# Optimization experiments

Measured on AMD Instinct MI355X. Metric: run time of the kernel, lower is better.

The kernel has to match this reference:

```python
import jax, jax.numpy as jnp
import numpy as np

T, B, OBS, ENC, H, A = 128, 256, 512, 256, 512, 18
N = T * B


def setup_inputs() -> dict:
    key = jax.random.key(0)
    ks = jax.random.split(key, 16)
    s = 0.02
    return {
        "x": jax.random.normal(ks[0], (N, OBS), jnp.float32),
        "gru_state": jax.random.normal(ks[1], (1, B, H), jnp.float32),
        "done": (jax.random.uniform(ks[2], (N,)) < 0.05).astype(jnp.float32),
        "action": jax.random.randint(ks[3], (N,), 0, A),
        # encoder MLP
        "w1": jax.random.normal(ks[4], (ENC, OBS), jnp.float32) * s,
        "b1": jnp.zeros((ENC,), jnp.float32),
        "w2": jax.random.normal(ks[5], (ENC, ENC), jnp.float32) * s,
        "b2": jnp.zeros((ENC,), jnp.float32),
        # GRU (PyTorch layout: gates [r, z, n] stacked along dim 0)
        "w_ih": jax.random.normal(ks[6], (3 * H, ENC), jnp.float32) * s,
        "w_hh": jax.random.normal(ks[7], (3 * H, H), jnp.float32) * s,
        "b_ih": jnp.zeros((3 * H,), jnp.float32),
        "b_hh": jnp.zeros((3 * H,), jnp.float32),
        # heads
        "w_actor": jax.random.normal(ks[8], (A, H), jnp.float32) * 0.01,
        "b_actor": jnp.zeros((A,), jnp.float32),
        "w_critic": jax.random.normal(ks[9], (1, H), jnp.float32) * s,
        "b_critic": jnp.zeros((1,), jnp.float32),
    }


def _gru_agent(x, gru_state, done, action, w1, b1, w2, b2, w_ih, w_hh, b_ih, b_hh,
               w_actor, b_actor, w_critic, b_critic):
    # MLP encoder
    h = jax.nn.relu(x @ w1.T + b1)
    h = jax.nn.relu(h @ w2.T + b2)  # (N, ENC)
    b = gru_state.shape[1]
    hs = h.reshape(-1, b, h.shape[-1])      # (T, B, ENC)
    dn = done.reshape(-1, b)                # (T, B)
    # precompute input-side gates for all timesteps: (T, B, 3H)
    gx = jnp.einsum('tbi,gi->tbg', hs, w_ih) + b_ih

    def step(h_prev, inp):
        gx_t, d_t = inp
        h_prev = h_prev * (1.0 - d_t)[:, None]   # done-based reset
        gh = h_prev @ w_hh.T + b_hh
        xr, xz, xn = jnp.split(gx_t, 3, axis=-1)
        hr, hz, hn = jnp.split(gh, 3, axis=-1)
        r = jax.nn.sigmoid(xr + hr)
        z = jax.nn.sigmoid(xz + hz)
        n = jnp.tanh(xn + r * hn)
        h_new = (1.0 - z) * n + z * h_prev
        return h_new, h_new

    h_last, outs = jax.lax.scan(step, gru_state[0], (gx, dn))
    hidden = outs.reshape(-1, outs.shape[-1])   # (N, H)

    logits = hidden @ w_actor.T + b_actor
    logp = jax.nn.log_softmax(logits, axis=-1)
    log_prob = jnp.take_along_axis(logp, action[:, None], axis=1)[:, 0]
    entropy = -jnp.sum(jnp.exp(logp) * logp, axis=-1)
    value = hidden @ w_critic.T + b_critic       # (N, 1)
    return log_prob, entropy, value, h_last[None]


def reference(x, gru_state, done, action, w1, b1, w2, b2, w_ih, w_hh, b_ih, b_hh,
              w_actor, b_actor, w_critic, b_critic):
    return _gru_agent(x, gru_state, done, action, w1, b1, w2, b2, w_ih, w_hh,
                      b_ih, b_hh, w_actor, b_actor, w_critic, b_critic)
```

## Files before the change

kernel.cpp:

```cpp
#include <hip/hip_runtime.h>
#include <hip/hip_bf16.h>

typedef short bf16x8 __attribute__((ext_vector_type(8)));
typedef float f32x4 __attribute__((ext_vector_type(4)));
typedef unsigned short u16;
typedef unsigned int u32;
typedef unsigned long long u64;

#define AS1 __attribute__((address_space(1)))
#define AS3 __attribute__((address_space(3)))

__device__ __forceinline__ u16 f2bf(float f) {
    __hip_bfloat16 h = __float2bfloat16(f);
    u16 r;
    __builtin_memcpy(&r, &h, 2);
    return r;
}
__device__ __forceinline__ float bf2f(u16 u) {
    u32 v = ((u32)u) << 16;
    float f;
    __builtin_memcpy(&f, &v, 4);
    return f;
}


constexpr int NW1  = 256 * 512;
constexpr int NW2  = 256 * 256;
constexpr int NWIH = 1536 * 256;

__global__ __launch_bounds__(256) void prep_kernel(
    const float* __restrict__ w1, const float* __restrict__ w2,
    const float* __restrict__ wih, const float* __restrict__ wact,
    const float* __restrict__ wcrit,
    u16* __restrict__ w1b, u16* __restrict__ w2b,
    u16* __restrict__ wihb, u16* __restrict__ wcatb) {
    long long gid = (long long)blockIdx.x * 256 + threadIdx.x;
    long long i4 = gid * 4;
    const float* src;
    u16* dst;
    if (i4 < NW1) { src = w1; dst = w1b; }
    else if ((i4 -= NW1) < NW2) { src = w2; dst = w2b; }
    else if ((i4 -= NW2) < NWIH) { src = wih; dst = wihb; }
    else {
        i4 -= NWIH;
        #pragma unroll
        for (int e = 0; e < 4; e++) {
            long long idx = i4 + e;
            int row = (int)(idx >> 9), col = (int)(idx & 511);
            float v = (row < 18) ? wact[row * 512 + col]
                    : (row == 18 ? wcrit[col] : 0.f);
            wcatb[idx] = f2bf(v);
        }
        return;
    }
    float4 v = *reinterpret_cast<const float4*>(src + i4);
    uint2 p;
    p.x = (u32)f2bf(v.x) | ((u32)f2bf(v.y) << 16);
    p.y = (u32)f2bf(v.z) | ((u32)f2bf(v.w) << 16);
    *reinterpret_cast<uint2*>(dst + i4) = p;
}

__global__ __launch_bounds__(256) void gemm_a32_bt_kernel(
    const float* __restrict__ A, const u16* __restrict__ B,
    const float* __restrict__ bias, u16* __restrict__ out,
    int M, int N, int K) {
    __shared__ u16 As[128 * 64];
    __shared__ u16 Bs[128 * 64];
    int tid = threadIdx.x;
    int lane = tid & 63, wave = tid >> 6;
    int m16 = lane & 15, quad = lane >> 4;
    int nb = N >> 7;
    int bm = blockIdx.x / nb, bn = blockIdx.x % nb;
    int wm = wave >> 1, wn = wave & 1;

    f32x4 acc[4][4];
    #pragma unroll
    for (int i = 0; i < 4; i++)
        #pragma unroll
        for (int j = 0; j < 4; j++) acc[i][j] = (f32x4){0.f, 0.f, 0.f, 0.f};

    const int rbase = wave * 32 + (lane >> 3);
    const int cpr = lane & 7;
    const int ar = tid >> 1, ah = (tid & 1) * 32;
    int kiters = K >> 6;
    for (int kb = 0; kb < kiters; kb++) {
        #pragma unroll
        for (int i = 0; i < 4; i++) {
            int r = rbase + i * 8;
            int cg = cpr ^ (r & 7);
            const u16* gb_ = B + (long long)(bn * 128 + r) * K + kb * 64 + cg * 8;
            __builtin_amdgcn_global_load_lds((const AS1 u32*)gb_, (AS3 u32*)&Bs[r * 64 + cpr * 8], 16, 0, 0);
        }
        const float* ga = A + (long long)(bm * 128 + ar) * K + kb * 64 + ah;
        #pragma unroll
        for (int g = 0; g < 4; g++) {
            float4 v0 = *reinterpret_cast<const float4*>(ga + g * 8);
            float4 v1 = *reinterpret_cast<const float4*>(ga + g * 8 + 4);
            uint4 pk;
            pk.x = (u32)f2bf(v0.x) | ((u32)f2bf(v0.y) << 16);
            pk.y = (u32)f2bf(v0.z) | ((u32)f2bf(v0.w) << 16);
            pk.z = (u32)f2bf(v1.x) | ((u32)f2bf(v1.y) << 16);
            pk.w = (u32)f2bf(v1.z) | ((u32)f2bf(v1.w) << 16);
            int sc = ((ah >> 3) + g) ^ (ar & 7);
            *reinterpret_cast<uint4*>(&As[ar * 64 + sc * 8]) = pk;
        }
        __syncthreads();
        #pragma unroll
        for (int ks = 0; ks < 2; ks++) {
            bf16x8 af[4], bfr[4];
            int lc = ks * 4 + quad;
            #pragma unroll
            for (int mt = 0; mt < 4; mt++) {
                int m = wm * 64 + mt * 16 + m16;
                af[mt] = *reinterpret_cast<const bf16x8*>(&As[m * 64 + (lc ^ (m & 7)) * 8]);
            }
            #pragma unroll
            for (int nt = 0; nt < 4; nt++) {
                int n = wn * 64 + nt * 16 + m16;
                bfr[nt] = *reinterpret_cast<const bf16x8*>(&Bs[n * 64 + (lc ^ (n & 7)) * 8]);
            }
            #pragma unroll
            for (int mt = 0; mt < 4; mt++)
                #pragma unroll
                for (int nt = 0; nt < 4; nt++)
                    acc[mt][nt] = __builtin_amdgcn_mfma_f32_16x16x32_bf16(af[mt], bfr[nt], acc[mt][nt], 0, 0, 0);
        }
        __syncthreads();
    }
    #pragma unroll
    for (int nt = 0; nt < 4; nt++) {
        int n = bn * 128 + wn * 64 + nt * 16 + m16;
        float bv = bias[n];
        #pragma unroll
        for (int mt = 0; mt < 4; mt++) {
            #pragma unroll
            for (int i = 0; i < 4; i++) {
                int m = bm * 128 + wm * 64 + mt * 16 + quad * 4 + i;
                float v = acc[mt][nt][i] + bv;
                out[(long long)m * N + n] = f2bf(fmaxf(v, 0.f));
            }
        }
    }
}

__global__ __launch_bounds__(256) void gemm_bt_kernel(
    const u16* __restrict__ A, const u16* __restrict__ B,
    const float* __restrict__ bias, u16* __restrict__ out,
    int M, int N, int K, int mode) {
    __shared__ u16 As[128 * 64];
    __shared__ u16 Bs[128 * 64];
    int tid = threadIdx.x;
    int lane = tid & 63, wave = tid >> 6;
    int m16 = lane & 15, quad = lane >> 4;
    int nb = N >> 7;
    int bm = blockIdx.x / nb, bn = blockIdx.x % nb;
    int wm = wave >> 1, wn = wave & 1;

    f32x4 acc[4][4];
    #pragma unroll
    for (int i = 0; i < 4; i++)
        #pragma unroll
        for (int j = 0; j < 4; j++) acc[i][j] = (f32x4){0.f, 0.f, 0.f, 0.f};

    const int rbase = wave * 32 + (lane >> 3);
    const int cpr = lane & 7;
    int kiters = K >> 6;
    for (int kb = 0; kb < kiters; kb++) {
        #pragma unroll
        for (int i = 0; i < 4; i++) {
            int r = rbase + i * 8;
            int cg = cpr ^ (r & 7);
            const u16* ga = A + (long long)(bm * 128 + r) * K + kb * 64 + cg * 8;
            const u16* gb_ = B + (long long)(bn * 128 + r) * K + kb * 64 + cg * 8;
            __builtin_amdgcn_global_load_lds((const AS1 u32*)ga, (AS3 u32*)&As[r * 64 + cpr * 8], 16, 0, 0);
            __builtin_amdgcn_global_load_lds((const AS1 u32*)gb_, (AS3 u32*)&Bs[r * 64 + cpr * 8], 16, 0, 0);
        }
        __syncthreads();
        #pragma unroll
        for (int ks = 0; ks < 2; ks++) {
            bf16x8 af[4], bfr[4];
            int lc = ks * 4 + quad;
            #pragma unroll
            for (int mt = 0; mt < 4; mt++) {
                int m = wm * 64 + mt * 16 + m16;
                af[mt] = *reinterpret_cast<const bf16x8*>(&As[m * 64 + (lc ^ (m & 7)) * 8]);
            }
            #pragma unroll
            for (int nt = 0; nt < 4; nt++) {
                int n = wn * 64 + nt * 16 + m16;
                bfr[nt] = *reinterpret_cast<const bf16x8*>(&Bs[n * 64 + (lc ^ (n & 7)) * 8]);
            }
            #pragma unroll
            for (int mt = 0; mt < 4; mt++)
                #pragma unroll
                for (int nt = 0; nt < 4; nt++)
                    acc[mt][nt] = __builtin_amdgcn_mfma_f32_16x16x32_bf16(af[mt], bfr[nt], acc[mt][nt], 0, 0, 0);
        }
        __syncthreads();
    }
    if (mode == 0) {
        #pragma unroll
        for (int nt = 0; nt < 4; nt++) {
            int n = bn * 128 + wn * 64 + nt * 16 + m16;
            float bv = bias[n];
            #pragma unroll
            for (int mt = 0; mt < 4; mt++) {
                #pragma unroll
                for (int i = 0; i < 4; i++) {
                    int m = bm * 128 + wm * 64 + mt * 16 + quad * 4 + i;
                    float v = acc[mt][nt][i] + bv;
                    out[(long long)m * N + n] = f2bf(fmaxf(v, 0.f));
                }
            }
        }
    } else {
        #pragma unroll
        for (int nt = 0; nt < 4; nt++) {
            int n = bn * 128 + wn * 64 + nt * 16 + m16;
            float bv = bias[n];
            int gkind = n >> 9, gj = n & 511;
            int gu = gj >> 5;
            int gate_local = gkind * 32 + (gj & 31);
            #pragma unroll
            for (int mt = 0; mt < 4; mt++) {
                #pragma unroll
                for (int i = 0; i < 4; i++) {
                    int m = bm * 128 + wm * 64 + mt * 16 + quad * 4 + i;
                    int t = m >> 8, bg = m & 255;
                    long long dst = ((((long long)t * 16 + (bg >> 4)) * 16 + gu) * 16 + (bg & 15)) * 96 + gate_local;
                    out[dst] = f2bf(acc[mt][nt][i] + bv);
                }
            }
        }
    }
}

__global__ __launch_bounds__(256) void scan_kernel(
    const float* __restrict__ gru_state, const float* __restrict__ done,
    const float* __restrict__ w_hh, const float* __restrict__ b_hh,
    const u16* __restrict__ gx, u16* h_pub, u16* hidden,
    float* h_last, int* flags) {
    __shared__ u16 h_lds[16 * 520];
    __shared__ float partial[4][16][104];
    int tid = threadIdx.x;
    int lane = tid & 63, wave = tid >> 6;
    int m16 = lane & 15, quad = lane >> 4;
    int gb = blockIdx.x & 15, gu = blockIdx.x >> 4;

    bf16x8 wfrag[6][4];
    #pragma unroll
    for (int nt = 0; nt < 6; nt++) {
        int g = nt * 16 + m16;
        int row = (g >> 5) * 512 + gu * 32 + (g & 31);
        #pragma unroll
        for (int ks = 0; ks < 4; ks++) {
            int k0 = wave * 128 + ks * 32 + quad * 8;
            const float* wp = w_hh + row * 512 + k0;
            float4 v0 = *reinterpret_cast<const float4*>(wp);
            float4 v1 = *reinterpret_cast<const float4*>(wp + 4);
            bf16x8 f;
            f[0] = (short)f2bf(v0.x); f[1] = (short)f2bf(v0.y);
            f[2] = (short)f2bf(v0.z); f[3] = (short)f2bf(v0.w);
            f[4] = (short)f2bf(v1.x); f[5] = (short)f2bf(v1.y);
            f[6] = (short)f2bf(v1.z); f[7] = (short)f2bf(v1.w);
            wfrag[nt][ks] = f;
        }
    }
    int b_ = tid >> 4, jj = (tid & 15) * 2;
    int bglob = gb * 16 + b_;
    int unit = gu * 32 + jj;
    float bhr0 = b_hh[unit],        bhr1 = b_hh[unit + 1];
    float bhz0 = b_hh[512 + unit],  bhz1 = b_hh[512 + unit + 1];
    float bhn0 = b_hh[1024 + unit], bhn1 = b_hh[1024 + unit + 1];
    float hs0 = gru_state[bglob * 512 + unit];
    float hs1 = gru_state[bglob * 512 + unit + 1];

    {
        u32 p = (u32)f2bf(hs0) | ((u32)f2bf(hs1) << 16);
        u32* dst = (u32*)h_pub + (bglob * 512 + unit) / 2;
        __hip_atomic_store(dst, p, __ATOMIC_RELAXED, __HIP_MEMORY_SCOPE_AGENT);
    }
    __syncthreads();
    if (tid == 0)
        __hip_atomic_store(&flags[gb * 16 + gu], 1, __ATOMIC_RELAXED, __HIP_MEMORY_SCOPE_AGENT);

    const int fillcol = (tid & 15) * 32;
    for (int t = 0; t < 128; t++) {
        const u16* gxp = gx + ((size_t)((t * 16 + gb) * 16 + gu) * 16 + b_) * 96;
        u32 pr = *reinterpret_cast<const u32*>(gxp + jj);
        u32 pz = *reinterpret_cast<const u32*>(gxp + 32 + jj);
        u32 pn = *reinterpret_cast<const u32*>(gxp + 64 + jj);
        float grx = bf2f((u16)pr), gry = bf2f((u16)(pr >> 16));
        float gzx = bf2f((u16)pz), gzy = bf2f((u16)(pz >> 16));
        float gnx = bf2f((u16)pn), gny = bf2f((u16)(pn >> 16));
        float dne = done[t * 256 + bglob];

        if (tid < 16) {
            while (__hip_atomic_load(&flags[gb * 16 + tid], __ATOMIC_RELAXED, __HIP_MEMORY_SCOPE_AGENT) < t + 1) {}
        }
        __syncthreads();
        {
            const u64* src = (const u64*)(h_pub + (size_t)(t & 1) * (256 * 512)) + (bglob * 512 + fillcol) / 4;
            bool keep = dne < 0.5f;
            #pragma unroll
            for (int q = 0; q < 8; q++) {
                u64 v = __hip_atomic_load((u64*)(src + q), __ATOMIC_RELAXED, __HIP_MEMORY_SCOPE_AGENT);
                if (!keep) v = 0;
                *reinterpret_cast<u64*>(&h_lds[b_ * 520 + fillcol + q * 4]) = v;
            }
        }
        __syncthreads();
        f32x4 acc[6];
        #pragma unroll
        for (int nt = 0; nt < 6; nt++) acc[nt] = (f32x4){0.f, 0.f, 0.f, 0.f};
        #pragma unroll
        for (int ks = 0; ks < 4; ks++) {
            bf16x8 a = *reinterpret_cast<const bf16x8*>(&h_lds[m16 * 520 + wave * 128 + ks * 32 + quad * 8]);
            #pragma unroll
            for (int nt = 0; nt < 6; nt++)
                acc[nt] = __builtin_amdgcn_mfma_f32_16x16x32_bf16(a, wfrag[nt][ks], acc[nt], 0, 0, 0);
        }
        #pragma unroll
        for (int nt = 0; nt < 6; nt++)
            #pragma unroll
            for (int i = 0; i < 4; i++)
                partial[wave][quad * 4 + i][nt * 16 + m16] = acc[nt][i];
        __syncthreads();
        float sr0 = 0, sr1 = 0, sz0 = 0, sz1 = 0, sn0 = 0, sn1 = 0;
        #pragma unroll
        for (int w = 0; w < 4; w++) {
            const float* p = &partial[w][b_][0];
            float2 a0 = *reinterpret_cast<const float2*>(p + jj);
            float2 a1 = *reinterpret_cast<const float2*>(p + 32 + jj);
            float2 a2 = *reinterpret_cast<const float2*>(p + 64 + jj);
            sr0 += a0.x; sr1 += a0.y;
            sz0 += a1.x; sz1 += a1.y;
            sn0 += a2.x; sn1 += a2.y;
        }
        float scale = 1.f - dne;
        hs0 *= scale; hs1 *= scale;
        float r0 = 1.f / (1.f + __expf(-(grx + sr0 + bhr0)));
        float r1 = 1.f / (1.f + __expf(-(gry + sr1 + bhr1)));
        float z0 = 1.f / (1.f + __expf(-(gzx + sz0 + bhz0)));
        float z1 = 1.f / (1.f + __expf(-(gzy + sz1 + bhz1)));
        float pn0 = gnx + r0 * (sn0 + bhn0);
        float pn1 = gny + r1 * (sn1 + bhn1);
        float n0 = 1.f - 2.f / (__expf(2.f * pn0) + 1.f);
        float n1 = 1.f - 2.f / (__expf(2.f * pn1) + 1.f);
        hs0 = (1.f - z0) * n0 + z0 * hs0;
        hs1 = (1.f - z1) * n1 + z1 * hs1;
        u32 packed = (u32)f2bf(hs0) | ((u32)f2bf(hs1) << 16);
        ((u32*)hidden)[((long long)(t * 256 + bglob) * 512 + unit) / 2] = packed;
        if (t < 127) {
            u32* dst = (u32*)(h_pub + (size_t)((t + 1) & 1) * (256 * 512)) + (bglob * 512 + unit) / 2;
            __hip_atomic_store(dst, packed, __ATOMIC_RELAXED, __HIP_MEMORY_SCOPE_AGENT);
        } else {
            h_last[bglob * 512 + unit] = hs0;
            h_last[bglob * 512 + unit + 1] = hs1;
        }
        __syncthreads();
        if (tid == 0 && t < 127)
            __hip_atomic_store(&flags[gb * 16 + gu], t + 2, __ATOMIC_RELAXED, __HIP_MEMORY_SCOPE_AGENT);
    }
}

__global__ __launch_bounds__(256) void heads_kernel(
    const u16* __restrict__ hidden, const u16* __restrict__ wcat,
    const float* __restrict__ b_actor, const float* __restrict__ b_critic,
    const int* __restrict__ action, float* __restrict__ out) {
    __shared__ float cls[4][16][34];
    int tid = threadIdx.x, lane = tid & 63, wave = tid >> 6;
    int m16 = lane & 15, quad = lane >> 4;
    int r0 = (blockIdx.x * 4 + wave) * 16;
    f32x4 acc0 = (f32x4){0.f, 0.f, 0.f, 0.f}, acc1 = (f32x4){0.f, 0.f, 0.f, 0.f};
    #pragma unroll
    for (int ks = 0; ks < 16; ks++) {
        bf16x8 a = *reinterpret_cast<const bf16x8*>(&hidden[(long long)(r0 + m16) * 512 + ks * 32 + quad * 8]);
        bf16x8 b0 = *reinterpret_cast<const bf16x8*>(&wcat[m16 * 512 + ks * 32 + quad * 8]);
        bf16x8 b1 = *reinterpret_cast<const bf16x8*>(&wcat[(16 + m16) * 512 + ks * 32 + quad * 8]);
        acc0 = __builtin_amdgcn_mfma_f32_16x16x32_bf16(a, b0, acc0, 0, 0, 0);
        acc1 = __builtin_amdgcn_mfma_f32_16x16x32_bf16(a, b1, acc1, 0, 0, 0);
    }
    #pragma unroll
    for (int i = 0; i < 4; i++) {
        cls[wave][quad * 4 + i][m16] = acc0[i];
        cls[wave][quad * 4 + i][16 + m16] = acc1[i];
    }
    __syncthreads();
    if (lane < 16) {
        int row = r0 + lane;
        float lg[18];
        float mx = -1e30f;
        #pragma unroll
        for (int a2 = 0; a2 < 18; a2++) {
            lg[a2] = cls[wave][lane][a2] + b_actor[a2];
            mx = fmaxf(mx, lg[a2]);
        }
        float s = 0.f, sl = 0.f;
        #pragma unroll
        for (int a2 = 0; a2 < 18; a2++) {
            float e = __expf(lg[a2] - mx);
            s += e; sl += e * lg[a2];
        }
        float logZ = mx + __logf(s);
        int act = action[row];
        float la = 0.f;
        #pragma unroll
        for (int a2 = 0; a2 < 18; a2++)
            if (a2 == act) la = lg[a2];
        out[row] = la - logZ;
        out[32768 + row] = logZ - sl / s;
        out[65536 + row] = cls[wave][lane][18] + b_critic[0];
    }
}

extern "C" void kernel_launch(void* const* d_in, const int* in_sizes, int n_in,
                              void* d_out, int out_size, void* d_ws, size_t ws_size,
                              hipStream_t stream) {
    const float* x        = (const float*)d_in[0];
    const float* gru_st   = (const float*)d_in[1];
    const float* done     = (const float*)d_in[2];
    const int*   action   = (const int*)d_in[3];
    const float* w1       = (const float*)d_in[4];
    const float* b1       = (const float*)d_in[5];
    const float* w2       = (const float*)d_in[6];
    const float* b2       = (const float*)d_in[7];
    const float* w_ih     = (const float*)d_in[8];
    const float* w_hh     = (const float*)d_in[9];
    const float* b_ih     = (const float*)d_in[10];
    const float* b_hh     = (const float*)d_in[11];
    const float* w_actor  = (const float*)d_in[12];
    const float* b_actor  = (const float*)d_in[13];
    const float* w_critic = (const float*)d_in[14];
    const float* b_critic = (const float*)d_in[15];
    float* out = (float*)d_out;

    char* ws = (char*)d_ws;
    u16* h1     = (u16*)(ws + 0LL);
    u16* h2     = (u16*)(ws + 16777216LL);
    u16* hidden = (u16*)(ws + 0LL);
    u16* w1b    = (u16*)(ws + 33554432LL);
    u16* w2b    = (u16*)(ws + 33816576LL);
    u16* wihb   = (u16*)(ws + 33947648LL);
    u16* wcatb  = (u16*)(ws + 34734080LL);
    u16* h_pub  = (u16*)(ws + 34766848LL);
    int* flags  = (int*)(ws + 35291136LL);
    u16* gxb    = (u16*)(ws + 37748736LL);
    float* h_last = out + 3 * 32768;

    hipMemsetAsync(flags, 0, 16 * 16 * 4, stream);
    prep_kernel<<<592, 256, 0, stream>>>(w1, w2, w_ih, w_actor, w_critic,
                                         w1b, w2b, wihb, wcatb);
    gemm_a32_bt_kernel<<<512, 256, 0, stream>>>(x, w1b, b1, h1, 32768, 256, 512);
    gemm_bt_kernel<<<512, 256, 0, stream>>>(h1, w2b, b2, h2, 32768, 256, 256, 0);
    gemm_bt_kernel<<<3072, 256, 0, stream>>>(h2, wihb, b_ih, gxb, 32768, 1536, 256, 1);

    void* args[] = {(void*)&gru_st, (void*)&done, (void*)&w_hh, (void*)&b_hh,
                    (void*)&gxb, (void*)&h_pub, (void*)&hidden, (void*)&h_last,
                    (void*)&flags};
    hipLaunchCooperativeKernel((void*)scan_kernel, dim3(256), dim3(256), args, 0, stream);

    heads_kernel<<<512, 256, 0, stream>>>(hidden, wcatb, b_actor, b_critic, action, out);
}
```

Baseline: 667.3 us.

## Tag published hidden state with step number, drop flag spin and LDS staging

Each published bf16 pair of hidden state now goes out as a 64-bit word whose upper half holds the timestep. Consumer waves spin directly on their own MFMA A-fragment words until every tag matches, then feed the data straight into MFMA registers. This removes the per-block flag array, its memset, the LDS staging buffer and two of the block barriers per step. The partial-sum buffer is double-buffered so the barrier at the end of each step can go. The cost is twice the bytes published and polled per step, and every lane now polls global memory instead of one thread per block.

```diff
diff --git a/kernel.cpp b/kernel.cpp
--- a/kernel.cpp
+++ b/kernel.cpp
@@ -238,10 +238,9 @@
 __global__ __launch_bounds__(256) void scan_kernel(
     const float* __restrict__ gru_state, const float* __restrict__ done,
     const float* __restrict__ w_hh, const float* __restrict__ b_hh,
-    const u16* __restrict__ gx, u16* h_pub, u16* hidden,
-    float* h_last, int* flags) {
-    __shared__ u16 h_lds[16 * 520];
-    __shared__ float partial[4][16][104];
+    const u16* __restrict__ gx, u64* h_pub, u16* hidden,
+    float* h_last) {
+    __shared__ float partial[2][4][16][98];
     int tid = threadIdx.x;
     int lane = tid & 63, wave = tid >> 6;
     int m16 = lane & 15, quad = lane >> 4;
@@ -277,14 +276,13 @@
 
     {
         u32 p = (u32)f2bf(hs0) | ((u32)f2bf(hs1) << 16);
-        u32* dst = (u32*)h_pub + (bglob * 512 + unit) / 2;
-        __hip_atomic_store(dst, p, __ATOMIC_RELAXED, __HIP_MEMORY_SCOPE_AGENT);
-    }
-    __syncthreads();
-    if (tid == 0)
-        __hip_atomic_store(&flags[gb * 16 + gu], 1, __ATOMIC_RELAXED, __HIP_MEMORY_SCOPE_AGENT);
-
-    const int fillcol = (tid & 15) * 32;
+        u64 pub = ((u64)1 << 32) | (u64)p;
+        __hip_atomic_store(h_pub + (size_t)bglob * 256 + (unit >> 1), pub,
+                           __ATOMIC_RELAXED, __HIP_MEMORY_SCOPE_AGENT);
+    }
+
+    const size_t rowoff = (size_t)(gb * 16 + m16) * 256 + (size_t)wave * 64 + quad * 4;
+
     for (int t = 0; t < 128; t++) {
         const u16* gxp = gx + ((size_t)((t * 16 + gb) * 16 + gu) * 16 + b_) * 96;
         u32 pr = *reinterpret_cast<const u32*>(gxp + jj);
@@ -294,42 +292,53 @@
         float gzx = bf2f((u16)pz), gzy = bf2f((u16)(pz >> 16));
         float gnx = bf2f((u16)pn), gny = bf2f((u16)(pn >> 16));
         float dne = done[t * 256 + bglob];
-
-        if (tid < 16) {
-            while (__hip_atomic_load(&flags[gb * 16 + tid], __ATOMIC_RELAXED, __HIP_MEMORY_SCOPE_AGENT) < t + 1) {}
-        }
-        __syncthreads();
-        {
-            const u64* src = (const u64*)(h_pub + (size_t)(t & 1) * (256 * 512)) + (bglob * 512 + fillcol) / 4;
-            bool keep = dne < 0.5f;
-            #pragma unroll
-            for (int q = 0; q < 8; q++) {
-                u64 v = __hip_atomic_load((u64*)(src + q), __ATOMIC_RELAXED, __HIP_MEMORY_SCOPE_AGENT);
-                if (!keep) v = 0;
-                *reinterpret_cast<u64*>(&h_lds[b_ * 520 + fillcol + q * 4]) = v;
-            }
-        }
-        __syncthreads();
+        float dnr = done[t * 256 + gb * 16 + m16];
+
+        u64* rowp = h_pub + (size_t)(t & 1) * 65536 + rowoff;
+        u64 e[4][4];
+        const u32 want = (u32)(t + 1);
+        for (;;) {
+            #pragma unroll
+            for (int ks = 0; ks < 4; ks++)
+                #pragma unroll
+                for (int j = 0; j < 4; j++)
+                    e[ks][j] = __hip_atomic_load(rowp + ks * 16 + j,
+                                                 __ATOMIC_RELAXED, __HIP_MEMORY_SCOPE_AGENT);
+            int mine = 1;
+            #pragma unroll
+            for (int ks = 0; ks < 4; ks++)
+                #pragma unroll
+                for (int j = 0; j < 4; j++)
+                    mine &= ((u32)(e[ks][j] >> 32) == want);
+            if (__all(mine)) break;
+        }
+        bool zrow = dnr >= 0.5f;
+        bf16x8 af[4];
+        #pragma unroll
+        for (int ks = 0; ks < 4; ks++) {
+            union { u32 w[4]; bf16x8 v; } u;
+            #pragma unroll
+            for (int j = 0; j < 4; j++) u.w[j] = zrow ? 0u : (u32)e[ks][j];
+            af[ks] = u.v;
+        }
         f32x4 acc[6];
         #pragma unroll
         for (int nt = 0; nt < 6; nt++) acc[nt] = (f32x4){0.f, 0.f, 0.f, 0.f};
         #pragma unroll
-        for (int ks = 0; ks < 4; ks++) {
-            bf16x8 a = *reinterpret_cast<const bf16x8*>(&h_lds[m16 * 520 + wave * 128 + ks * 32 + quad * 8]);
+        for (int ks = 0; ks < 4; ks++)
             #pragma unroll
             for (int nt = 0; nt < 6; nt++)
-                acc[nt] = __builtin_amdgcn_mfma_f32_16x16x32_bf16(a, wfrag[nt][ks], acc[nt], 0, 0, 0);
-        }
+                acc[nt] = __builtin_amdgcn_mfma_f32_16x16x32_bf16(af[ks], wfrag[nt][ks], acc[nt], 0, 0, 0);
         #pragma unroll
         for (int nt = 0; nt < 6; nt++)
             #pragma unroll
             for (int i = 0; i < 4; i++)
-                partial[wave][quad * 4 + i][nt * 16 + m16] = acc[nt][i];
+                partial[t & 1][wave][quad * 4 + i][nt * 16 + m16] = acc[nt][i];
         __syncthreads();
         float sr0 = 0, sr1 = 0, sz0 = 0, sz1 = 0, sn0 = 0, sn1 = 0;
         #pragma unroll
         for (int w = 0; w < 4; w++) {
-            const float* p = &partial[w][b_][0];
+            const float* p = &partial[t & 1][w][b_][0];
             float2 a0 = *reinterpret_cast<const float2*>(p + jj);
             float2 a1 = *reinterpret_cast<const float2*>(p + 32 + jj);
             float2 a2 = *reinterpret_cast<const float2*>(p + 64 + jj);
@@ -350,17 +359,16 @@
         hs0 = (1.f - z0) * n0 + z0 * hs0;
         hs1 = (1.f - z1) * n1 + z1 * hs1;
         u32 packed = (u32)f2bf(hs0) | ((u32)f2bf(hs1) << 16);
-        ((u32*)hidden)[((long long)(t * 256 + bglob) * 512 + unit) / 2] = packed;
         if (t < 127) {
-            u32* dst = (u32*)(h_pub + (size_t)((t + 1) & 1) * (256 * 512)) + (bglob * 512 + unit) / 2;
-            __hip_atomic_store(dst, packed, __ATOMIC_RELAXED, __HIP_MEMORY_SCOPE_AGENT);
+            u64 pub = ((u64)(u32)(t + 2) << 32) | (u64)packed;
+            __hip_atomic_store(h_pub + (size_t)((t + 1) & 1) * 65536 +
+                               (size_t)bglob * 256 + (unit >> 1), pub,
+                               __ATOMIC_RELAXED, __HIP_MEMORY_SCOPE_AGENT);
         } else {
             h_last[bglob * 512 + unit] = hs0;
             h_last[bglob * 512 + unit + 1] = hs1;
         }
-        __syncthreads();
-        if (tid == 0 && t < 127)
-            __hip_atomic_store(&flags[gb * 16 + gu], t + 2, __ATOMIC_RELAXED, __HIP_MEMORY_SCOPE_AGENT);
+        ((u32*)hidden)[((long long)(t * 256 + bglob) * 512 + unit) / 2] = packed;
     }
 }
 
@@ -443,12 +451,10 @@
     u16* w2b    = (u16*)(ws + 33816576LL);
     u16* wihb   = (u16*)(ws + 33947648LL);
     u16* wcatb  = (u16*)(ws + 34734080LL);
-    u16* h_pub  = (u16*)(ws + 34766848LL);
-    int* flags  = (int*)(ws + 35291136LL);
+    u64* h_pub  = (u64*)(ws + 34766848LL);
     u16* gxb    = (u16*)(ws + 37748736LL);
     float* h_last = out + 3 * 32768;
 
-    hipMemsetAsync(flags, 0, 16 * 16 * 4, stream);
     prep_kernel<<<592, 256, 0, stream>>>(w1, w2, w_ih, w_actor, w_critic,
                                          w1b, w2b, wihb, wcatb);
     gemm_a32_bt_kernel<<<512, 256, 0, stream>>>(x, w1b, b1, h1, 32768, 256, 512);
@@ -456,8 +462,7 @@
     gemm_bt_kernel<<<3072, 256, 0, stream>>>(h2, wihb, b_ih, gxb, 32768, 1536, 256, 1);
 
     void* args[] = {(void*)&gru_st, (void*)&done, (void*)&w_hh, (void*)&b_hh,
-                    (void*)&gxb, (void*)&h_pub, (void*)&hidden, (void*)&h_last,
-                    (void*)&flags};
+                    (void*)&gxb, (void*)&h_pub, (void*)&hidden, (void*)&h_last};
     hipLaunchCooperativeKernel((void*)scan_kernel, dim3(256), dim3(256), args, 0, stream);
 
     heads_kernel<<<512, 256, 0, stream>>>(hidden, wcatb, b_actor, b_critic, action, out);
```

New measurement: 761.9 us. 1.14x slower.

## Replace per-block barrier flags with per-wave flags in GRU scan

Applied to the files above, without the earlier changes.

Each wave now publishes its own progress flag right after its hidden-state stores drain, and every lane polls one of the 64 per-wave flags for its batch group. This removes the block-wide barriers around publish and poll on the serial per-timestep path. The hidden output store moves after the flag publish, and the partial buffer padding changes. Dropping barriers risks LDS reuse hazards between waves if no other barrier protects h_lds.

```diff
diff --git a/kernel.cpp b/kernel.cpp
--- a/kernel.cpp
+++ b/kernel.cpp
@@ -238,10 +238,10 @@
 __global__ __launch_bounds__(256) void scan_kernel(
     const float* __restrict__ gru_state, const float* __restrict__ done,
     const float* __restrict__ w_hh, const float* __restrict__ b_hh,
-    const u16* __restrict__ gx, u16* h_pub, u16* hidden,
-    float* h_last, int* flags) {
+    const u16* __restrict__ gx, u16* h_pub, u32* flags, u16* hidden,
+    float* h_last) {
     __shared__ u16 h_lds[16 * 520];
-    __shared__ float partial[4][16][104];
+    __shared__ float partial[4][16][98];
     int tid = threadIdx.x;
     int lane = tid & 63, wave = tid >> 6;
     int m16 = lane & 15, quad = lane >> 4;
@@ -280,9 +280,10 @@
         u32* dst = (u32*)h_pub + (bglob * 512 + unit) / 2;
         __hip_atomic_store(dst, p, __ATOMIC_RELAXED, __HIP_MEMORY_SCOPE_AGENT);
     }
-    __syncthreads();
-    if (tid == 0)
-        __hip_atomic_store(&flags[gb * 16 + gu], 1, __ATOMIC_RELAXED, __HIP_MEMORY_SCOPE_AGENT);
+    __builtin_amdgcn_s_waitcnt(0x0f70);
+    if (lane == 0)
+        __hip_atomic_store(&flags[gb * 64 + gu * 4 + wave], 1u,
+                           __ATOMIC_RELAXED, __HIP_MEMORY_SCOPE_AGENT);
 
     const int fillcol = (tid & 15) * 32;
     for (int t = 0; t < 128; t++) {
@@ -295,10 +296,10 @@
         float gnx = bf2f((u16)pn), gny = bf2f((u16)(pn >> 16));
         float dne = done[t * 256 + bglob];
 
-        if (tid < 16) {
-            while (__hip_atomic_load(&flags[gb * 16 + tid], __ATOMIC_RELAXED, __HIP_MEMORY_SCOPE_AGENT) < t + 1) {}
-        }
-        __syncthreads();
+        const u32 want = (u32)(t + 1);
+        while (__hip_atomic_load(&flags[gb * 64 + lane],
+                                 __ATOMIC_RELAXED, __HIP_MEMORY_SCOPE_AGENT) < want) {}
+
         {
             const u64* src = (const u64*)(h_pub + (size_t)(t & 1) * (256 * 512)) + (bglob * 512 + fillcol) / 4;
             bool keep = dne < 0.5f;
@@ -350,17 +351,18 @@
         hs0 = (1.f - z0) * n0 + z0 * hs0;
         hs1 = (1.f - z1) * n1 + z1 * hs1;
         u32 packed = (u32)f2bf(hs0) | ((u32)f2bf(hs1) << 16);
-        ((u32*)hidden)[((long long)(t * 256 + bglob) * 512 + unit) / 2] = packed;
         if (t < 127) {
             u32* dst = (u32*)(h_pub + (size_t)((t + 1) & 1) * (256 * 512)) + (bglob * 512 + unit) / 2;
             __hip_atomic_store(dst, packed, __ATOMIC_RELAXED, __HIP_MEMORY_SCOPE_AGENT);
+            __builtin_amdgcn_s_waitcnt(0x0f70);
+            if (lane == 0)
+                __hip_atomic_store(&flags[gb * 64 + gu * 4 + wave], (u32)(t + 2),
+                                   __ATOMIC_RELAXED, __HIP_MEMORY_SCOPE_AGENT);
         } else {
             h_last[bglob * 512 + unit] = hs0;
             h_last[bglob * 512 + unit + 1] = hs1;
         }
-        __syncthreads();
-        if (tid == 0 && t < 127)
-            __hip_atomic_store(&flags[gb * 16 + gu], t + 2, __ATOMIC_RELAXED, __HIP_MEMORY_SCOPE_AGENT);
+        ((u32*)hidden)[(size_t)(t * 256 + bglob) * 256 + (unit >> 1)] = packed;
     }
 }
 
@@ -444,11 +446,11 @@
     u16* wihb   = (u16*)(ws + 33947648LL);
     u16* wcatb  = (u16*)(ws + 34734080LL);
     u16* h_pub  = (u16*)(ws + 34766848LL);
-    int* flags  = (int*)(ws + 35291136LL);
+    u32* flags  = (u32*)(ws + 35291136LL);
     u16* gxb    = (u16*)(ws + 37748736LL);
     float* h_last = out + 3 * 32768;
 
-    hipMemsetAsync(flags, 0, 16 * 16 * 4, stream);
+    hipMemsetAsync(flags, 0, 16 * 64 * 4, stream);
     prep_kernel<<<592, 256, 0, stream>>>(w1, w2, w_ih, w_actor, w_critic,
                                          w1b, w2b, wihb, wcatb);
     gemm_a32_bt_kernel<<<512, 256, 0, stream>>>(x, w1b, b1, h1, 32768, 256, 512);
@@ -456,8 +458,8 @@
     gemm_bt_kernel<<<3072, 256, 0, stream>>>(h2, wihb, b_ih, gxb, 32768, 1536, 256, 1);
 
     void* args[] = {(void*)&gru_st, (void*)&done, (void*)&w_hh, (void*)&b_hh,
-                    (void*)&gxb, (void*)&h_pub, (void*)&hidden, (void*)&h_last,
-                    (void*)&flags};
+                    (void*)&gxb, (void*)&h_pub, (void*)&flags, (void*)&hidden,
+                    (void*)&h_last};
     hipLaunchCooperativeKernel((void*)scan_kernel, dim3(256), dim3(256), args, 0, stream);
 
     heads_kernel<<<512, 256, 0, stream>>>(hidden, wcatb, b_actor, b_critic, action, out);
```

Result: slower. 1.086 ms (+62.8%).
